# Performance work log

Hardware: AMD Instinct MI355X
Metric: run time of the kernel (lower is better)

Reference implementation:

```python
import jax, jax.numpy as jnp
import numpy as np
from jax import lax

INPUT_DIM = 16
H1 = 5
H2 = 50
NUM_CLASSES = 20
B = 4096
T = 512


def _lstm(x, w_ih, w_hh, b_ih, b_hh, hidden):
    # x: [B, T, D]; PyTorch LSTM gate order i, f, g, o; returns all hidden states [B, T, H]
    xg = jnp.einsum('btd,gd->btg', x, w_ih) + (b_ih + b_hh)  # [B, T, 4H]
    xg_t = jnp.swapaxes(xg, 0, 1)  # [T, B, 4H]
    h0 = jnp.zeros((x.shape[0], hidden), x.dtype)
    c0 = jnp.zeros((x.shape[0], hidden), x.dtype)

    def step(carry, xt):
        h, c = carry
        g = xt + h @ w_hh.T  # [B, 4H]
        i, f, gg, o = jnp.split(g, 4, axis=-1)
        i = jax.nn.sigmoid(i)
        f = jax.nn.sigmoid(f)
        gg = jnp.tanh(gg)
        o = jax.nn.sigmoid(o)
        c = f * c + i * gg
        h = o * jnp.tanh(c)
        return (h, c), h

    _, hs = lax.scan(step, (h0, c0), xg_t)
    return jnp.swapaxes(hs, 0, 1)  # [B, T, H]


def setup_inputs() -> dict:
    key = jax.random.key(0)
    ks = jax.random.split(key, 12)
    s1 = 1.0 / np.sqrt(H1)
    s2 = 1.0 / np.sqrt(H2)
    u = lambda k, shape, s: jax.random.uniform(k, shape, jnp.float32, -s, s)
    return {
        'x': jax.random.normal(ks[0], (B, T, INPUT_DIM), jnp.float32),
        'w_ih1': u(ks[1], (4 * H1, INPUT_DIM), s1),
        'w_hh1': u(ks[2], (4 * H1, H1), s1),
        'b_ih1': u(ks[3], (4 * H1,), s1),
        'b_hh1': u(ks[4], (4 * H1,), s1),
        'w_ih2': u(ks[5], (4 * H2, H1), s2),
        'w_hh2': u(ks[6], (4 * H2, H2), s2),
        'b_ih2': u(ks[7], (4 * H2,), s2),
        'b_hh2': u(ks[8], (4 * H2,), s2),
        'fc_w': u(ks[9], (NUM_CLASSES, H2), s2),
        'fc_b': u(ks[10], (NUM_CLASSES,), s2),
    }


def reference(x, w_ih1, w_hh1, b_ih1, b_hh1, w_ih2, w_hh2, b_ih2, b_hh2, fc_w, fc_b):
    h1 = _lstm(x, w_ih1, w_hh1, b_ih1, b_hh1, H1)   # [B, T, 5]
    h2 = _lstm(h1, w_ih2, w_hh2, b_ih2, b_hh2, H2)  # [B, T, 50]
    feat = h2[:, -1, :]  # last timestep; dropout is identity in eval mode
    out = feat @ fc_w.T + fc_b  # [B, num_classes]
    return (out, feat)
```

## Files before the change

### kernel.cpp

```cpp
#include <hip/hip_runtime.h>
#include <stdint.h>

#define B_TOTAL 4096
#define T_STEPS 512
#define IN_DIM 16
#define H1 5
#define H2 50
#define NCLS 20

typedef __attribute__((ext_vector_type(8))) short bf16x8;
typedef __attribute__((ext_vector_type(4))) float f32x4;

__device__ inline unsigned short f2bf(float x){
  unsigned int u = __float_as_uint(x);
  u += 0x7FFFu + ((u >> 16) & 1u);
  return (unsigned short)(u >> 16);
}
__device__ inline float bf2f(unsigned short h){ return __uint_as_float(((unsigned int)h) << 16); }

#define LOG2E 1.44269504f
__device__ inline float sigm(float x){
  float e = __builtin_amdgcn_exp2f(-LOG2E * x);
  return __builtin_amdgcn_rcpf(1.0f + e);
}
__device__ inline float tanh_(float x){
  float e = __builtin_amdgcn_exp2f((2.0f*LOG2E) * x);
  float r = __builtin_amdgcn_rcpf(1.0f + e);
  return fmaf(-2.0f, r, 1.0f);
}

__global__ __launch_bounds__(320) void lstm_fused_kernel(
    const float* __restrict__ x,
    const float* __restrict__ w_ih1, const float* __restrict__ w_hh1,
    const float* __restrict__ b_ih1, const float* __restrict__ b_hh1,
    const float* __restrict__ w_ih2, const float* __restrict__ w_hh2,
    const float* __restrict__ b_ih2, const float* __restrict__ b_hh2,
    const float* __restrict__ fc_w, const float* __restrict__ fc_b,
    float* __restrict__ out)
{
  const int tid  = threadIdx.x;
  const int lane = tid & 63;
  const int wave = tid >> 6;
  const int l15  = lane & 15;
  const int quad = lane >> 4;
  const int b0   = blockIdx.x * 16;

  __shared__ __align__(16) unsigned short a1_hi[2][16*40];
  __shared__ __align__(16) unsigned short a1_lo[2][16*40];
  __shared__ __align__(16) unsigned short a2_hi[2][16*72];
  __shared__ __align__(16) unsigned short a2_lo[2][16*72];
  __shared__ float h2f[16*52];

  bf16x8 Bh[4][2], Bl[4][2];
  float bias[4];
  float cst[4] = {0.f, 0.f, 0.f, 0.f};

  if (wave == 4) {
    bool valid = l15 < H1;
#pragma unroll
    for (int tt=0; tt<4; ++tt){
      int grow = tt*H1 + l15;
#pragma unroll
      for (int j=0;j<8;j++){
        int k = quad*8 + j;
        float w = 0.f;
        if (valid){
          if (k < IN_DIM)          w = w_ih1[grow*IN_DIM + k];
          else if (k < IN_DIM+H1)  w = w_hh1[grow*H1 + (k-IN_DIM)];
        }
        unsigned short h = f2bf(w), l = f2bf(w - bf2f(h));
        Bh[tt][0][j] = (short)h; Bl[tt][0][j] = (short)l;
        Bh[tt][1][j] = 0;        Bl[tt][1][j] = 0;
      }
      bias[tt] = valid ? (b_ih1[grow] + b_hh1[grow]) : 0.f;
    }
  } else {
    int cg = wave*16 + l15;
    bool valid = cg < H2;
#pragma unroll
    for (int tt=0; tt<4; ++tt){
      int grow = tt*H2 + cg;
#pragma unroll
      for (int kt=0; kt<2; ++kt){
#pragma unroll
        for (int j=0;j<8;j++){
          int k = kt*32 + quad*8 + j;
          float w = 0.f;
          if (valid){
            if (k < H2)          w = w_hh2[grow*H2 + k];
            else if (k < H2+H1)  w = w_ih2[grow*H1 + (k-H2)];
          }
          unsigned short h = f2bf(w), l = f2bf(w - bf2f(h));
          Bh[tt][kt][j] = (short)h; Bl[tt][kt][j] = (short)l;
        }
      }
      bias[tt] = valid ? (b_ih2[grow] + b_hh2[grow]) : 0.f;
    }
  }

  {
    unsigned short* p;
    p = &a1_hi[0][0]; for (int i=tid;i<2*16*40;i+=320) p[i]=0;
    p = &a1_lo[0][0]; for (int i=tid;i<2*16*40;i+=320) p[i]=0;
    p = &a2_hi[0][0]; for (int i=tid;i<2*16*72;i+=320) p[i]=0;
    p = &a2_lo[0][0]; for (int i=tid;i<2*16*72;i+=320) p[i]=0;
  }

  const int xb = lane >> 2;
  const int xd = (lane & 3) * 4;
  float4 xa = make_float4(0,0,0,0);
  if (wave == 4) {
    float4 x0 = *(const float4*)&x[((size_t)(b0+xb)*T_STEPS + 0)*IN_DIM + xd];
    uint2 uh, ul;
    unsigned short h0=f2bf(x0.x), h1v=f2bf(x0.y), h2v=f2bf(x0.z), h3=f2bf(x0.w);
    unsigned short l0=f2bf(x0.x-bf2f(h0)), l1=f2bf(x0.y-bf2f(h1v)),
                   l2=f2bf(x0.z-bf2f(h2v)), l3=f2bf(x0.w-bf2f(h3));
    uh.x = (unsigned)h0 | ((unsigned)h1v<<16); uh.y = (unsigned)h2v | ((unsigned)h3<<16);
    ul.x = (unsigned)l0 | ((unsigned)l1<<16);  ul.y = (unsigned)l2 | ((unsigned)l3<<16);
    *(uint2*)&a1_hi[0][xb*40 + xd] = uh;
    *(uint2*)&a1_lo[0][xb*40 + xd] = ul;
    xa = *(const float4*)&x[((size_t)(b0+xb)*T_STEPS + 1)*IN_DIM + xd];
  }

  for (int t=0; t<=T_STEPS; ++t){
    __syncthreads();
    const int rd = t & 1, wr = rd ^ 1;

    if (wave == 4){
      if (t < T_STEPS){
        float4 xn = make_float4(0,0,0,0);
        if (t+2 < T_STEPS)
          xn = *(const float4*)&x[((size_t)(b0+xb)*T_STEPS + (t+2))*IN_DIM + xd];

        bf16x8 ah = *(const bf16x8*)&a1_hi[rd][l15*40 + quad*8];
        bf16x8 al = *(const bf16x8*)&a1_lo[rd][l15*40 + quad*8];
        f32x4 acc[4];
#pragma unroll
        for (int tt=0; tt<4; ++tt){
          f32x4 a = {bias[tt], bias[tt], bias[tt], bias[tt]};
          a = __builtin_amdgcn_mfma_f32_16x16x32_bf16(ah, Bh[tt][0], a, 0,0,0);
          a = __builtin_amdgcn_mfma_f32_16x16x32_bf16(al, Bh[tt][0], a, 0,0,0);
          a = __builtin_amdgcn_mfma_f32_16x16x32_bf16(ah, Bl[tt][0], a, 0,0,0);
          acc[tt] = a;
        }
#pragma unroll
        for (int r=0;r<4;r++){
          float gi = sigm(acc[0][r]);
          float gf = sigm(acc[1][r]);
          float gg = tanh_(acc[2][r]);
          float go = sigm(acc[3][r]);
          cst[r] = gf*cst[r] + gi*gg;
          float h = go * tanh_(cst[r]);
          unsigned short hh = f2bf(h), hl = f2bf(h - bf2f(hh));
          int bb = quad*4 + r;
          if (l15 < H1){
            a1_hi[wr][bb*40 + IN_DIM + l15] = hh;
            a1_lo[wr][bb*40 + IN_DIM + l15] = hl;
            a2_hi[wr][bb*72 + H2 + l15] = hh;
            a2_lo[wr][bb*72 + H2 + l15] = hl;
          }
        }
        if (t+1 < T_STEPS){
          unsigned short h0=f2bf(xa.x), h1v=f2bf(xa.y), h2v=f2bf(xa.z), h3=f2bf(xa.w);
          unsigned short l0=f2bf(xa.x-bf2f(h0)), l1=f2bf(xa.y-bf2f(h1v)),
                         l2=f2bf(xa.z-bf2f(h2v)), l3=f2bf(xa.w-bf2f(h3));
          uint2 uh, ul;
          uh.x = (unsigned)h0 | ((unsigned)h1v<<16); uh.y = (unsigned)h2v | ((unsigned)h3<<16);
          ul.x = (unsigned)l0 | ((unsigned)l1<<16);  ul.y = (unsigned)l2 | ((unsigned)l3<<16);
          *(uint2*)&a1_hi[wr][xb*40 + xd] = uh;
          *(uint2*)&a1_lo[wr][xb*40 + xd] = ul;
        }
        xa = xn;
      }
    } else {
      if (t >= 1){
        const int cg = wave*16 + l15;
        bf16x8 ah0 = *(const bf16x8*)&a2_hi[rd][l15*72 +  0 + quad*8];
        bf16x8 al0 = *(const bf16x8*)&a2_lo[rd][l15*72 +  0 + quad*8];
        bf16x8 ah1 = *(const bf16x8*)&a2_hi[rd][l15*72 + 32 + quad*8];
        bf16x8 al1 = *(const bf16x8*)&a2_lo[rd][l15*72 + 32 + quad*8];
        f32x4 acc[4];
#pragma unroll
        for (int tt=0; tt<4; ++tt){
          f32x4 a = {bias[tt], bias[tt], bias[tt], bias[tt]};
          a = __builtin_amdgcn_mfma_f32_16x16x32_bf16(ah0, Bh[tt][0], a, 0,0,0);
          a = __builtin_amdgcn_mfma_f32_16x16x32_bf16(al0, Bh[tt][0], a, 0,0,0);
          a = __builtin_amdgcn_mfma_f32_16x16x32_bf16(ah0, Bl[tt][0], a, 0,0,0);
          a = __builtin_amdgcn_mfma_f32_16x16x32_bf16(ah1, Bh[tt][1], a, 0,0,0);
          a = __builtin_amdgcn_mfma_f32_16x16x32_bf16(al1, Bh[tt][1], a, 0,0,0);
          a = __builtin_amdgcn_mfma_f32_16x16x32_bf16(ah1, Bl[tt][1], a, 0,0,0);
          acc[tt] = a;
        }
#pragma unroll
        for (int r=0;r<4;r++){
          float gi = sigm(acc[0][r]);
          float gf = sigm(acc[1][r]);
          float gg = tanh_(acc[2][r]);
          float go = sigm(acc[3][r]);
          cst[r] = gf*cst[r] + gi*gg;
          float h = go * tanh_(cst[r]);
          unsigned short hh = f2bf(h), hl = f2bf(h - bf2f(hh));
          int bb = quad*4 + r;
          if (cg < H2){
            a2_hi[wr][bb*72 + cg] = hh;
            a2_lo[wr][bb*72 + cg] = hl;
            if (t == T_STEPS){
              out[(size_t)B_TOTAL*NCLS + (size_t)(b0+bb)*H2 + cg] = h;
              h2f[bb*52 + cg] = h;
            }
          }
        }
      }
    }
  }

  __syncthreads();
  {
    int b = tid / 20, o = tid % 20;
    float s = fc_b[o];
#pragma unroll 10
    for (int k=0;k<H2;k++) s += fc_w[o*H2+k] * h2f[b*52+k];
    out[(size_t)(b0+b)*NCLS + o] = s;
  }
}

extern "C" void kernel_launch(void* const* d_in, const int* in_sizes, int n_in,
                              void* d_out, int out_size, void* d_ws, size_t ws_size,
                              hipStream_t stream) {
  const float* x     = (const float*)d_in[0];
  const float* w_ih1 = (const float*)d_in[1];
  const float* w_hh1 = (const float*)d_in[2];
  const float* b_ih1 = (const float*)d_in[3];
  const float* b_hh1 = (const float*)d_in[4];
  const float* w_ih2 = (const float*)d_in[5];
  const float* w_hh2 = (const float*)d_in[6];
  const float* b_ih2 = (const float*)d_in[7];
  const float* b_hh2 = (const float*)d_in[8];
  const float* fc_w  = (const float*)d_in[9];
  const float* fc_b  = (const float*)d_in[10];
  float* out = (float*)d_out;

  lstm_fused_kernel<<<dim3(B_TOTAL/16), dim3(320), 0, stream>>>(
      x, w_ih1, w_hh1, b_ih1, b_hh1, w_ih2, w_hh2, b_ih2, b_hh2, fc_w, fc_b, out);
}
```

Baseline: 733.5 us.

## Split LSTM gate computation across 12 waves with two-phase barrier per step

Raises the block from 5 to 12 waves. Layer-2 gates are now split over two roles (i,f vs g,o) and layer-1 gates get one wave per gate, with activations exchanged through shared memory and two barriers per timestep instead of one double-buffered barrier. Input x is staged eight timesteps at a time into an LDS ring rather than loaded every step. Float-to-bf16 hi/lo splitting switches from round-to-nearest to truncation with byte-permute packing. The aim is a shorter per-step critical path on the serial recurrence, paid for by an extra barrier per step and more LDS traffic.

```diff
diff --git a/kernel.cpp b/kernel.cpp
--- a/kernel.cpp
+++ b/kernel.cpp
@@ -11,13 +11,6 @@
 typedef __attribute__((ext_vector_type(8))) short bf16x8;
 typedef __attribute__((ext_vector_type(4))) float f32x4;
 
-__device__ inline unsigned short f2bf(float x){
-  unsigned int u = __float_as_uint(x);
-  u += 0x7FFFu + ((u >> 16) & 1u);
-  return (unsigned short)(u >> 16);
-}
-__device__ inline float bf2f(unsigned short h){ return __uint_as_float(((unsigned int)h) << 16); }
-
 #define LOG2E 1.44269504f
 __device__ inline float sigm(float x){
   float e = __builtin_amdgcn_exp2f(-LOG2E * x);
@@ -28,8 +21,31 @@
   float r = __builtin_amdgcn_rcpf(1.0f + e);
   return fmaf(-2.0f, r, 1.0f);
 }
-
-__global__ __launch_bounds__(320) void lstm_fused_kernel(
+__device__ inline unsigned pack_top(float a, float b){
+  return __builtin_amdgcn_perm(__float_as_uint(a), __float_as_uint(b), 0x07060302u);
+}
+__device__ inline void cvt_store(unsigned short* dh, unsigned short* dl, float4 v){
+  unsigned x0=__float_as_uint(v.x), x1=__float_as_uint(v.y),
+           x2=__float_as_uint(v.z), x3=__float_as_uint(v.w);
+  uint2 H, L;
+  H.x = pack_top(v.y, v.x);
+  H.y = pack_top(v.w, v.z);
+  float r0 = v.x - __uint_as_float(x0 & 0xFFFF0000u);
+  float r1 = v.y - __uint_as_float(x1 & 0xFFFF0000u);
+  float r2 = v.z - __uint_as_float(x2 & 0xFFFF0000u);
+  float r3 = v.w - __uint_as_float(x3 & 0xFFFF0000u);
+  L.x = pack_top(r1, r0);
+  L.y = pack_top(r3, r2);
+  *(uint2*)dh = H; *(uint2*)dl = L;
+}
+__device__ inline void split1(float h, unsigned short& hi, unsigned short& lo){
+  unsigned u = __float_as_uint(h);
+  hi = (unsigned short)(u >> 16);
+  float r = h - __uint_as_float(u & 0xFFFF0000u);
+  lo = (unsigned short)(__float_as_uint(r) >> 16);
+}
+
+__global__ __launch_bounds__(768) void lstm_fused_kernel(
     const float* __restrict__ x,
     const float* __restrict__ w_ih1, const float* __restrict__ w_hh1,
     const float* __restrict__ b_ih1, const float* __restrict__ b_hh1,
@@ -45,177 +61,244 @@
   const int quad = lane >> 4;
   const int b0   = blockIdx.x * 16;
 
-  __shared__ __align__(16) unsigned short a1_hi[2][16*40];
-  __shared__ __align__(16) unsigned short a1_lo[2][16*40];
-  __shared__ __align__(16) unsigned short a2_hi[2][16*72];
-  __shared__ __align__(16) unsigned short a2_lo[2][16*72];
+  __shared__ __align__(16) unsigned short a2h[16*72], a2l[16*72];
+  __shared__ __align__(16) unsigned short a1h[16*24], a1l[16*24];
+  __shared__ __align__(16) unsigned short xrh[8*16*24], xrl[8*16*24];
+  __shared__ float g2[2*16*68];
+  __shared__ float g1[3*16*8 + 16];
   __shared__ float h2f[16*52];
 
-  bf16x8 Bh[4][2], Bl[4][2];
-  float bias[4];
-  float cst[4] = {0.f, 0.f, 0.f, 0.f};
-
-  if (wave == 4) {
-    bool valid = l15 < H1;
-#pragma unroll
-    for (int tt=0; tt<4; ++tt){
-      int grow = tt*H1 + l15;
-#pragma unroll
-      for (int j=0;j<8;j++){
-        int k = quad*8 + j;
-        float w = 0.f;
-        if (valid){
-          if (k < IN_DIM)          w = w_ih1[grow*IN_DIM + k];
-          else if (k < IN_DIM+H1)  w = w_hh1[grow*H1 + (k-IN_DIM)];
-        }
-        unsigned short h = f2bf(w), l = f2bf(w - bf2f(h));
-        Bh[tt][0][j] = (short)h; Bl[tt][0][j] = (short)l;
-        Bh[tt][1][j] = 0;        Bl[tt][1][j] = 0;
-      }
-      bias[tt] = valid ? (b_ih1[grow] + b_hh1[grow]) : 0.f;
-    }
-  } else {
-    int cg = wave*16 + l15;
+  bf16x8 Bh[2][2], Bl[2][2];
+  float bias0 = 0.f, bias1 = 0.f;
+  const bool is2  = wave < 8;
+  const int  grp  = wave & 3;
+  const int  role = wave >> 2;
+  const int  cg   = grp*16 + l15;
+
+  if (is2){
     bool valid = cg < H2;
 #pragma unroll
-    for (int tt=0; tt<4; ++tt){
+    for (int tl=0; tl<2; ++tl){
+      int tt = role*2 + tl;
       int grow = tt*H2 + cg;
 #pragma unroll
       for (int kt=0; kt<2; ++kt){
 #pragma unroll
         for (int j=0;j<8;j++){
-          int k = kt*32 + quad*8 + j;
+          int kk = kt*32 + quad*8 + j;
           float w = 0.f;
           if (valid){
-            if (k < H2)          w = w_hh2[grow*H2 + k];
-            else if (k < H2+H1)  w = w_ih2[grow*H1 + (k-H2)];
-          }
-          unsigned short h = f2bf(w), l = f2bf(w - bf2f(h));
-          Bh[tt][kt][j] = (short)h; Bl[tt][kt][j] = (short)l;
-        }
-      }
-      bias[tt] = valid ? (b_ih2[grow] + b_hh2[grow]) : 0.f;
-    }
+            if (kk < H2)         w = w_hh2[grow*H2 + kk];
+            else if (kk < H2+H1) w = w_ih2[grow*H1 + (kk-H2)];
+          }
+          unsigned u = __float_as_uint(w);
+          Bh[tl][kt][j] = (short)(u >> 16);
+          float r = w - __uint_as_float(u & 0xFFFF0000u);
+          Bl[tl][kt][j] = (short)(__float_as_uint(r) >> 16);
+        }
+      }
+      float bv = valid ? (b_ih2[grow] + b_hh2[grow]) : 0.f;
+      if (tl==0) bias0 = bv; else bias1 = bv;
+    }
+  } else {
+    int tt = wave & 3;
+    bool valid = l15 < H1;
+    int grow = tt*H1 + l15;
+#pragma unroll
+    for (int j=0;j<8;j++){
+      int kk = quad*8 + j;
+      float w = 0.f;
+      if (valid){
+        if (kk < IN_DIM)             w = w_ih1[grow*IN_DIM + kk];
+        else if (kk < IN_DIM+H1)     w = w_hh1[grow*H1 + (kk-IN_DIM)];
+      }
+      unsigned u = __float_as_uint(w);
+      Bh[0][0][j] = (short)(u >> 16);
+      float r = w - __uint_as_float(u & 0xFFFF0000u);
+      Bl[0][0][j] = (short)(__float_as_uint(r) >> 16);
+      Bh[0][1][j] = 0; Bl[0][1][j] = 0;
+      Bh[1][0][j] = 0; Bl[1][0][j] = 0;
+      Bh[1][1][j] = 0; Bl[1][1][j] = 0;
+    }
+    bias0 = valid ? (b_ih1[grow] + b_hh1[grow]) : 0.f;
   }
 
-  {
-    unsigned short* p;
-    p = &a1_hi[0][0]; for (int i=tid;i<2*16*40;i+=320) p[i]=0;
-    p = &a1_lo[0][0]; for (int i=tid;i<2*16*40;i+=320) p[i]=0;
-    p = &a2_hi[0][0]; for (int i=tid;i<2*16*72;i+=320) p[i]=0;
-    p = &a2_lo[0][0]; for (int i=tid;i<2*16*72;i+=320) p[i]=0;
-  }
+  for (int i=tid;i<16*72;i+=768){ a2h[i]=0; a2l[i]=0; }
+  for (int i=tid;i<16*24;i+=768){ a1h[i]=0; a1l[i]=0; }
 
   const int xb = lane >> 2;
   const int xd = (lane & 3) * 4;
-  float4 xa = make_float4(0,0,0,0);
-  if (wave == 4) {
-    float4 x0 = *(const float4*)&x[((size_t)(b0+xb)*T_STEPS + 0)*IN_DIM + xd];
-    uint2 uh, ul;
-    unsigned short h0=f2bf(x0.x), h1v=f2bf(x0.y), h2v=f2bf(x0.z), h3=f2bf(x0.w);
-    unsigned short l0=f2bf(x0.x-bf2f(h0)), l1=f2bf(x0.y-bf2f(h1v)),
-                   l2=f2bf(x0.z-bf2f(h2v)), l3=f2bf(x0.w-bf2f(h3));
-    uh.x = (unsigned)h0 | ((unsigned)h1v<<16); uh.y = (unsigned)h2v | ((unsigned)h3<<16);
-    ul.x = (unsigned)l0 | ((unsigned)l1<<16);  ul.y = (unsigned)l2 | ((unsigned)l3<<16);
-    *(uint2*)&a1_hi[0][xb*40 + xd] = uh;
-    *(uint2*)&a1_lo[0][xb*40 + xd] = ul;
-    xa = *(const float4*)&x[((size_t)(b0+xb)*T_STEPS + 1)*IN_DIM + xd];
+  if (wave == 10){
+#pragma unroll
+    for (int s=0;s<8;s++){
+      float4 v = *(const float4*)&x[((size_t)(b0+xb)*T_STEPS + s)*IN_DIM + xd];
+      cvt_store(&xrh[(s*16+xb)*24+xd], &xrl[(s*16+xb)*24+xd], v);
+    }
   }
+  __syncthreads();
+
+  float cst[4] = {0.f,0.f,0.f,0.f};
+  float x7x=0.f, x7y=0.f, x7z=0.f, x7w=0.f;
 
   for (int t=0; t<=T_STEPS; ++t){
+    f32x4 acc0 = {0,0,0,0}, acc1 = {0,0,0,0};
+    bool reload = false;
+
+    if (is2){
+      if (t >= 1){
+        const int rb = l15*72;
+        bf16x8 ah0 = *(const bf16x8*)&a2h[rb +      quad*8];
+        bf16x8 al0 = *(const bf16x8*)&a2l[rb +      quad*8];
+        bf16x8 ah1 = *(const bf16x8*)&a2h[rb + 32 + quad*8];
+        bf16x8 al1 = *(const bf16x8*)&a2l[rb + 32 + quad*8];
+        acc0 = (f32x4){bias0,bias0,bias0,bias0};
+        acc0 = __builtin_amdgcn_mfma_f32_16x16x32_bf16(ah0, Bh[0][0], acc0, 0,0,0);
+        acc0 = __builtin_amdgcn_mfma_f32_16x16x32_bf16(al0, Bh[0][0], acc0, 0,0,0);
+        acc0 = __builtin_amdgcn_mfma_f32_16x16x32_bf16(ah0, Bl[0][0], acc0, 0,0,0);
+        acc0 = __builtin_amdgcn_mfma_f32_16x16x32_bf16(ah1, Bh[0][1], acc0, 0,0,0);
+        acc0 = __builtin_amdgcn_mfma_f32_16x16x32_bf16(al1, Bh[0][1], acc0, 0,0,0);
+        acc0 = __builtin_amdgcn_mfma_f32_16x16x32_bf16(ah1, Bl[0][1], acc0, 0,0,0);
+        acc1 = (f32x4){bias1,bias1,bias1,bias1};
+        acc1 = __builtin_amdgcn_mfma_f32_16x16x32_bf16(ah0, Bh[1][0], acc1, 0,0,0);
+        acc1 = __builtin_amdgcn_mfma_f32_16x16x32_bf16(al0, Bh[1][0], acc1, 0,0,0);
+        acc1 = __builtin_amdgcn_mfma_f32_16x16x32_bf16(ah0, Bl[1][0], acc1, 0,0,0);
+        acc1 = __builtin_amdgcn_mfma_f32_16x16x32_bf16(ah1, Bh[1][1], acc1, 0,0,0);
+        acc1 = __builtin_amdgcn_mfma_f32_16x16x32_bf16(al1, Bh[1][1], acc1, 0,0,0);
+        acc1 = __builtin_amdgcn_mfma_f32_16x16x32_bf16(ah1, Bl[1][1], acc1, 0,0,0);
+        if (role == 0){
+#pragma unroll
+          for (int r=0;r<4;r++){ acc0[r] = sigm(acc0[r]); acc1[r] = sigm(acc1[r]); }
+        } else {
+#pragma unroll
+          for (int r=0;r<4;r++){
+            float g = tanh_(acc0[r]);
+            float o = sigm(acc1[r]);
+            int row = quad*4 + r;
+            g2[       row*68 + cg] = g;
+            g2[1088 + row*68 + cg] = o;
+          }
+        }
+      }
+    } else {
+      if (t < T_STEPS){
+        float4 xv0,xv1,xv2,xv3,xv4,xv5,xv6,xv7;
+        reload = (wave==10) && ((t & 7) == 7) && (t < T_STEPS-8);
+        if (reload){
+          const float* xp = &x[((size_t)(b0+xb)*T_STEPS + (t+1))*IN_DIM + xd];
+          xv0 = *(const float4*)(xp +  0*IN_DIM);
+          xv1 = *(const float4*)(xp +  1*IN_DIM);
+          xv2 = *(const float4*)(xp +  2*IN_DIM);
+          xv3 = *(const float4*)(xp +  3*IN_DIM);
+          xv4 = *(const float4*)(xp +  4*IN_DIM);
+          xv5 = *(const float4*)(xp +  5*IN_DIM);
+          xv6 = *(const float4*)(xp +  6*IN_DIM);
+          xv7 = *(const float4*)(xp +  7*IN_DIM);
+        }
+        const int slot = t & 7;
+        const unsigned short* ph;
+        const unsigned short* pl;
+        if (quad < 2){
+          int off = (slot*16 + l15)*24 + quad*8;
+          ph = &xrh[off]; pl = &xrl[off];
+        } else {
+          int off = l15*24 + (quad-2)*8;
+          ph = &a1h[off]; pl = &a1l[off];
+        }
+        bf16x8 ah = *(const bf16x8*)ph;
+        bf16x8 al = *(const bf16x8*)pl;
+        acc0 = (f32x4){bias0,bias0,bias0,bias0};
+        acc0 = __builtin_amdgcn_mfma_f32_16x16x32_bf16(ah, Bh[0][0], acc0, 0,0,0);
+        acc0 = __builtin_amdgcn_mfma_f32_16x16x32_bf16(al, Bh[0][0], acc0, 0,0,0);
+        acc0 = __builtin_amdgcn_mfma_f32_16x16x32_bf16(ah, Bl[0][0], acc0, 0,0,0);
+        int tt = wave & 3;
+        if (wave == 8){
+#pragma unroll
+          for (int r=0;r<4;r++) acc0[r] = sigm(acc0[r]);
+        } else {
+#pragma unroll
+          for (int r=0;r<4;r++){
+            float v = (tt==2) ? tanh_(acc0[r]) : sigm(acc0[r]);
+            if (l15 < 8) g1[(tt-1)*128 + (quad*4+r)*8 + l15] = v;
+          }
+        }
+        if (reload){
+          int base = ((t+1) & 7); (void)base;
+          cvt_store(&xrh[(0*16+xb)*24+xd], &xrl[(0*16+xb)*24+xd], xv0);
+          cvt_store(&xrh[(1*16+xb)*24+xd], &xrl[(1*16+xb)*24+xd], xv1);
+          cvt_store(&xrh[(2*16+xb)*24+xd], &xrl[(2*16+xb)*24+xd], xv2);
+          cvt_store(&xrh[(3*16+xb)*24+xd], &xrl[(3*16+xb)*24+xd], xv3);
+          cvt_store(&xrh[(4*16+xb)*24+xd], &xrl[(4*16+xb)*24+xd], xv4);
+          cvt_store(&xrh[(5*16+xb)*24+xd], &xrl[(5*16+xb)*24+xd], xv5);
+          cvt_store(&xrh[(6*16+xb)*24+xd], &xrl[(6*16+xb)*24+xd], xv6);
+          x7x = xv7.x; x7y = xv7.y; x7z = xv7.z; x7w = xv7.w;
+        }
+      }
+    }
+
     __syncthreads();
-    const int rd = t & 1, wr = rd ^ 1;
-
-    if (wave == 4){
-      if (t < T_STEPS){
-        float4 xn = make_float4(0,0,0,0);
-        if (t+2 < T_STEPS)
-          xn = *(const float4*)&x[((size_t)(b0+xb)*T_STEPS + (t+2))*IN_DIM + xd];
-
-        bf16x8 ah = *(const bf16x8*)&a1_hi[rd][l15*40 + quad*8];
-        bf16x8 al = *(const bf16x8*)&a1_lo[rd][l15*40 + quad*8];
-        f32x4 acc[4];
-#pragma unroll
-        for (int tt=0; tt<4; ++tt){
-          f32x4 a = {bias[tt], bias[tt], bias[tt], bias[tt]};
-          a = __builtin_amdgcn_mfma_f32_16x16x32_bf16(ah, Bh[tt][0], a, 0,0,0);
-          a = __builtin_amdgcn_mfma_f32_16x16x32_bf16(al, Bh[tt][0], a, 0,0,0);
-          a = __builtin_amdgcn_mfma_f32_16x16x32_bf16(ah, Bl[tt][0], a, 0,0,0);
-          acc[tt] = a;
-        }
+
+    if (is2){
+      if (role == 0 && t >= 1){
+        float gg[4], go[4];
 #pragma unroll
         for (int r=0;r<4;r++){
-          float gi = sigm(acc[0][r]);
-          float gf = sigm(acc[1][r]);
-          float gg = tanh_(acc[2][r]);
-          float go = sigm(acc[3][r]);
-          cst[r] = gf*cst[r] + gi*gg;
-          float h = go * tanh_(cst[r]);
-          unsigned short hh = f2bf(h), hl = f2bf(h - bf2f(hh));
-          int bb = quad*4 + r;
+          int row = quad*4 + r;
+          gg[r] = g2[       row*68 + cg];
+          go[r] = g2[1088 + row*68 + cg];
+        }
+#pragma unroll
+        for (int r=0;r<4;r++){
+          cst[r] = acc1[r]*cst[r] + acc0[r]*gg[r];
+          float h = go[r] * tanh_(cst[r]);
+          int row = quad*4 + r;
+          if (cg < H2){
+            unsigned short hh, hl;
+            split1(h, hh, hl);
+            a2h[row*72 + cg] = hh;
+            a2l[row*72 + cg] = hl;
+            if (t == T_STEPS){
+              out[(size_t)B_TOTAL*NCLS + (size_t)(b0+row)*H2 + cg] = h;
+              h2f[row*52 + cg] = h;
+            }
+          }
+        }
+      }
+    } else if (t < T_STEPS){
+      if (wave == 8){
+        int cc = (l15 < H1) ? l15 : 0;
+        float gf[4], gg[4], go[4];
+#pragma unroll
+        for (int r=0;r<4;r++){
+          int row = quad*4 + r;
+          gf[r] = g1[0*128 + row*8 + cc];
+          gg[r] = g1[1*128 + row*8 + cc];
+          go[r] = g1[2*128 + row*8 + cc];
+        }
+#pragma unroll
+        for (int r=0;r<4;r++){
+          cst[r] = gf[r]*cst[r] + acc0[r]*gg[r];
+          float h = go[r] * tanh_(cst[r]);
+          int row = quad*4 + r;
           if (l15 < H1){
-            a1_hi[wr][bb*40 + IN_DIM + l15] = hh;
-            a1_lo[wr][bb*40 + IN_DIM + l15] = hl;
-            a2_hi[wr][bb*72 + H2 + l15] = hh;
-            a2_lo[wr][bb*72 + H2 + l15] = hl;
-          }
-        }
-        if (t+1 < T_STEPS){
-          unsigned short h0=f2bf(xa.x), h1v=f2bf(xa.y), h2v=f2bf(xa.z), h3=f2bf(xa.w);
-          unsigned short l0=f2bf(xa.x-bf2f(h0)), l1=f2bf(xa.y-bf2f(h1v)),
-                         l2=f2bf(xa.z-bf2f(h2v)), l3=f2bf(xa.w-bf2f(h3));
-          uint2 uh, ul;
-          uh.x = (unsigned)h0 | ((unsigned)h1v<<16); uh.y = (unsigned)h2v | ((unsigned)h3<<16);
-          ul.x = (unsigned)l0 | ((unsigned)l1<<16);  ul.y = (unsigned)l2 | ((unsigned)l3<<16);
-          *(uint2*)&a1_hi[wr][xb*40 + xd] = uh;
-          *(uint2*)&a1_lo[wr][xb*40 + xd] = ul;
-        }
-        xa = xn;
-      }
-    } else {
-      if (t >= 1){
-        const int cg = wave*16 + l15;
-        bf16x8 ah0 = *(const bf16x8*)&a2_hi[rd][l15*72 +  0 + quad*8];
-        bf16x8 al0 = *(const bf16x8*)&a2_lo[rd][l15*72 +  0 + quad*8];
-        bf16x8 ah1 = *(const bf16x8*)&a2_hi[rd][l15*72 + 32 + quad*8];
-        bf16x8 al1 = *(const bf16x8*)&a2_lo[rd][l15*72 + 32 + quad*8];
-        f32x4 acc[4];
-#pragma unroll
-        for (int tt=0; tt<4; ++tt){
-          f32x4 a = {bias[tt], bias[tt], bias[tt], bias[tt]};
-          a = __builtin_amdgcn_mfma_f32_16x16x32_bf16(ah0, Bh[tt][0], a, 0,0,0);
-          a = __builtin_amdgcn_mfma_f32_16x16x32_bf16(al0, Bh[tt][0], a, 0,0,0);
-          a = __builtin_amdgcn_mfma_f32_16x16x32_bf16(ah0, Bl[tt][0], a, 0,0,0);
-          a = __builtin_amdgcn_mfma_f32_16x16x32_bf16(ah1, Bh[tt][1], a, 0,0,0);
-          a = __builtin_amdgcn_mfma_f32_16x16x32_bf16(al1, Bh[tt][1], a, 0,0,0);
-          a = __builtin_amdgcn_mfma_f32_16x16x32_bf16(ah1, Bl[tt][1], a, 0,0,0);
-          acc[tt] = a;
-        }
-#pragma unroll
-        for (int r=0;r<4;r++){
-          float gi = sigm(acc[0][r]);
-          float gf = sigm(acc[1][r]);
-          float gg = tanh_(acc[2][r]);
-          float go = sigm(acc[3][r]);
-          cst[r] = gf*cst[r] + gi*gg;
-          float h = go * tanh_(cst[r]);
-          unsigned short hh = f2bf(h), hl = f2bf(h - bf2f(hh));
-          int bb = quad*4 + r;
-          if (cg < H2){
-            a2_hi[wr][bb*72 + cg] = hh;
-            a2_lo[wr][bb*72 + cg] = hl;
-            if (t == T_STEPS){
-              out[(size_t)B_TOTAL*NCLS + (size_t)(b0+bb)*H2 + cg] = h;
-              h2f[bb*52 + cg] = h;
-            }
-          }
-        }
-      }
-    }
+            unsigned short hh, hl;
+            split1(h, hh, hl);
+            a1h[row*24 + cc] = hh;
+            a1l[row*24 + cc] = hl;
+            a2h[row*72 + H2 + cc] = hh;
+            a2l[row*72 + H2 + cc] = hl;
+          }
+        }
+      }
+      if (reload){
+        float4 v; v.x=x7x; v.y=x7y; v.z=x7z; v.w=x7w;
+        cvt_store(&xrh[(7*16+xb)*24+xd], &xrl[(7*16+xb)*24+xd], v);
+      }
+    }
+
+    __syncthreads();
   }
 
-  __syncthreads();
-  {
+  if (tid < 320){
     int b = tid / 20, o = tid % 20;
     float s = fc_b[o];
 #pragma unroll 10
@@ -240,6 +323,6 @@
   const float* fc_b  = (const float*)d_in[10];
   float* out = (float*)d_out;
 
-  lstm_fused_kernel<<<dim3(B_TOTAL/16), dim3(320), 0, stream>>>(
+  lstm_fused_kernel<<<dim3(B_TOTAL/16), dim3(768), 0, stream>>>(
       x, w_ih1, w_hh1, b_ih1, b_hh1, w_ih2, w_hh2, b_ih2, b_hh2, fc_w, fc_b, out);
 }
```

New measurement: 749.2 us. 2.1% more time.

## Replace per-step block barriers with LDS counter spin-waits between LSTM layer waves

Applied to the files above, without the earlier changes.

Replaces the per-timestep __syncthreads with producer/consumer LDS atomic counters, so the layer-1 wave and the layer-2 waves synchronize point-to-point and can run up to a step apart. Input x is now prefetched four steps at a time into an 8-slot LDS ring. bf16 hi/lo splitting switches from round-to-nearest to truncation via byte permutes. MFMA accumulations are split into two independent chains to shorten the dependency latency. The aim is less barrier stall and conversion ALU work on the serial recurrence path, at the cost of spin-loop overhead, subtle memory-ordering risk, and a slight change in rounding.

```diff
diff --git a/kernel.cpp b/kernel.cpp
--- a/kernel.cpp
+++ b/kernel.cpp
@@ -11,13 +11,6 @@
 typedef __attribute__((ext_vector_type(8))) short bf16x8;
 typedef __attribute__((ext_vector_type(4))) float f32x4;
 
-__device__ inline unsigned short f2bf(float x){
-  unsigned int u = __float_as_uint(x);
-  u += 0x7FFFu + ((u >> 16) & 1u);
-  return (unsigned short)(u >> 16);
-}
-__device__ inline float bf2f(unsigned short h){ return __uint_as_float(((unsigned int)h) << 16); }
-
 #define LOG2E 1.44269504f
 __device__ inline float sigm(float x){
   float e = __builtin_amdgcn_exp2f(-LOG2E * x);
@@ -28,8 +21,39 @@
   float r = __builtin_amdgcn_rcpf(1.0f + e);
   return fmaf(-2.0f, r, 1.0f);
 }
-
-__global__ __launch_bounds__(320) void lstm_fused_kernel(
+__device__ inline unsigned pack_top(float a, float b){
+  return __builtin_amdgcn_perm(__float_as_uint(a), __float_as_uint(b), 0x07060302u);
+}
+__device__ inline void cvt_store(unsigned short* dh, unsigned short* dl, float4 v){
+  uint2 H, L;
+  H.x = pack_top(v.y, v.x);
+  H.y = pack_top(v.w, v.z);
+  float r0 = v.x - __uint_as_float(__float_as_uint(v.x) & 0xFFFF0000u);
+  float r1 = v.y - __uint_as_float(__float_as_uint(v.y) & 0xFFFF0000u);
+  float r2 = v.z - __uint_as_float(__float_as_uint(v.z) & 0xFFFF0000u);
+  float r3 = v.w - __uint_as_float(__float_as_uint(v.w) & 0xFFFF0000u);
+  L.x = pack_top(r1, r0);
+  L.y = pack_top(r3, r2);
+  *(uint2*)dh = H; *(uint2*)dl = L;
+}
+__device__ inline void split1(float h, unsigned short& hi, unsigned short& lo){
+  unsigned u = __float_as_uint(h);
+  hi = (unsigned short)(u >> 16);
+  float r = h - __uint_as_float(u & 0xFFFF0000u);
+  lo = (unsigned short)(__float_as_uint(r) >> 16);
+}
+__device__ inline void wsplit(float w, short& hi, short& lo){
+  unsigned u = __float_as_uint(w);
+  hi = (short)(u >> 16);
+  float r = w - __uint_as_float(u & 0xFFFF0000u);
+  lo = (short)(__float_as_uint(r) >> 16);
+}
+__device__ inline void spin_ge(unsigned* p, unsigned tgt){
+  while (__hip_atomic_load(p, __ATOMIC_ACQUIRE, __HIP_MEMORY_SCOPE_WORKGROUP) < tgt)
+    __builtin_amdgcn_s_sleep(1);
+}
+
+__global__ __launch_bounds__(320, 1) void lstm_fused_kernel(
     const float* __restrict__ x,
     const float* __restrict__ w_ih1, const float* __restrict__ w_hh1,
     const float* __restrict__ b_ih1, const float* __restrict__ b_hh1,
@@ -45,172 +69,184 @@
   const int quad = lane >> 4;
   const int b0   = blockIdx.x * 16;
 
-  __shared__ __align__(16) unsigned short a1_hi[2][16*40];
-  __shared__ __align__(16) unsigned short a1_lo[2][16*40];
-  __shared__ __align__(16) unsigned short a2_hi[2][16*72];
-  __shared__ __align__(16) unsigned short a2_lo[2][16*72];
+  __shared__ __align__(16) unsigned short a2h[2][16*72], a2l[2][16*72];
+  __shared__ __align__(16) unsigned short xrh[8][16*24], xrl[8][16*24];
+  __shared__ __align__(16) unsigned short a1h[16*24], a1l[16*24];
   __shared__ float h2f[16*52];
+  __shared__ unsigned cnt1, cnt2;
 
   bf16x8 Bh[4][2], Bl[4][2];
   float bias[4];
-  float cst[4] = {0.f, 0.f, 0.f, 0.f};
-
-  if (wave == 4) {
+  float cst[4] = {0.f,0.f,0.f,0.f};
+  const int cg = wave*16 + l15;
+
+  if (wave < 4){
+    bool valid = cg < H2;
+#pragma unroll
+    for (int tt=0; tt<4; ++tt){
+      int grow = tt*H2 + cg;
+#pragma unroll
+      for (int kt=0; kt<2; ++kt){
+#pragma unroll
+        for (int j=0;j<8;j++){
+          int kk = kt*32 + quad*8 + j;
+          float w = 0.f;
+          if (valid){
+            if (kk < H2)         w = w_hh2[grow*H2 + kk];
+            else if (kk < H2+H1) w = w_ih2[grow*H1 + (kk-H2)];
+          }
+          short hi, lo; wsplit(w, hi, lo);
+          Bh[tt][kt][j] = hi; Bl[tt][kt][j] = lo;
+        }
+      }
+      bias[tt] = valid ? (b_ih2[grow] + b_hh2[grow]) : 0.f;
+    }
+  } else {
     bool valid = l15 < H1;
 #pragma unroll
     for (int tt=0; tt<4; ++tt){
       int grow = tt*H1 + l15;
 #pragma unroll
       for (int j=0;j<8;j++){
-        int k = quad*8 + j;
+        int kk = quad*8 + j;
         float w = 0.f;
         if (valid){
-          if (k < IN_DIM)          w = w_ih1[grow*IN_DIM + k];
-          else if (k < IN_DIM+H1)  w = w_hh1[grow*H1 + (k-IN_DIM)];
-        }
-        unsigned short h = f2bf(w), l = f2bf(w - bf2f(h));
-        Bh[tt][0][j] = (short)h; Bl[tt][0][j] = (short)l;
-        Bh[tt][1][j] = 0;        Bl[tt][1][j] = 0;
+          if (kk < IN_DIM)         w = w_ih1[grow*IN_DIM + kk];
+          else if (kk < IN_DIM+H1) w = w_hh1[grow*H1 + (kk-IN_DIM)];
+        }
+        short hi, lo; wsplit(w, hi, lo);
+        Bh[tt][0][j] = hi; Bl[tt][0][j] = lo;
+        Bh[tt][1][j] = 0;  Bl[tt][1][j] = 0;
       }
       bias[tt] = valid ? (b_ih1[grow] + b_hh1[grow]) : 0.f;
     }
-  } else {
-    int cg = wave*16 + l15;
-    bool valid = cg < H2;
-#pragma unroll
-    for (int tt=0; tt<4; ++tt){
-      int grow = tt*H2 + cg;
-#pragma unroll
-      for (int kt=0; kt<2; ++kt){
-#pragma unroll
-        for (int j=0;j<8;j++){
-          int k = kt*32 + quad*8 + j;
-          float w = 0.f;
-          if (valid){
-            if (k < H2)          w = w_hh2[grow*H2 + k];
-            else if (k < H2+H1)  w = w_ih2[grow*H1 + (k-H2)];
-          }
-          unsigned short h = f2bf(w), l = f2bf(w - bf2f(h));
-          Bh[tt][kt][j] = (short)h; Bl[tt][kt][j] = (short)l;
-        }
-      }
-      bias[tt] = valid ? (b_ih2[grow] + b_hh2[grow]) : 0.f;
-    }
-  }
-
-  {
-    unsigned short* p;
-    p = &a1_hi[0][0]; for (int i=tid;i<2*16*40;i+=320) p[i]=0;
-    p = &a1_lo[0][0]; for (int i=tid;i<2*16*40;i+=320) p[i]=0;
-    p = &a2_hi[0][0]; for (int i=tid;i<2*16*72;i+=320) p[i]=0;
-    p = &a2_lo[0][0]; for (int i=tid;i<2*16*72;i+=320) p[i]=0;
-  }
+  }
+
+  { unsigned short* p = &a2h[0][0]; for (int i=tid;i<2*16*72;i+=320) p[i]=0; }
+  { unsigned short* p = &a2l[0][0]; for (int i=tid;i<2*16*72;i+=320) p[i]=0; }
+  { unsigned short* p = &a1h[0];    for (int i=tid;i<16*24;i+=320)   p[i]=0; }
+  { unsigned short* p = &a1l[0];    for (int i=tid;i<16*24;i+=320)   p[i]=0; }
+  if (tid == 0){ cnt1 = 0; cnt2 = 0; }
 
   const int xb = lane >> 2;
   const int xd = (lane & 3) * 4;
-  float4 xa = make_float4(0,0,0,0);
-  if (wave == 4) {
-    float4 x0 = *(const float4*)&x[((size_t)(b0+xb)*T_STEPS + 0)*IN_DIM + xd];
-    uint2 uh, ul;
-    unsigned short h0=f2bf(x0.x), h1v=f2bf(x0.y), h2v=f2bf(x0.z), h3=f2bf(x0.w);
-    unsigned short l0=f2bf(x0.x-bf2f(h0)), l1=f2bf(x0.y-bf2f(h1v)),
-                   l2=f2bf(x0.z-bf2f(h2v)), l3=f2bf(x0.w-bf2f(h3));
-    uh.x = (unsigned)h0 | ((unsigned)h1v<<16); uh.y = (unsigned)h2v | ((unsigned)h3<<16);
-    ul.x = (unsigned)l0 | ((unsigned)l1<<16);  ul.y = (unsigned)l2 | ((unsigned)l3<<16);
-    *(uint2*)&a1_hi[0][xb*40 + xd] = uh;
-    *(uint2*)&a1_lo[0][xb*40 + xd] = ul;
-    xa = *(const float4*)&x[((size_t)(b0+xb)*T_STEPS + 1)*IN_DIM + xd];
-  }
-
-  for (int t=0; t<=T_STEPS; ++t){
-    __syncthreads();
-    const int rd = t & 1, wr = rd ^ 1;
-
-    if (wave == 4){
-      if (t < T_STEPS){
-        float4 xn = make_float4(0,0,0,0);
-        if (t+2 < T_STEPS)
-          xn = *(const float4*)&x[((size_t)(b0+xb)*T_STEPS + (t+2))*IN_DIM + xd];
-
-        bf16x8 ah = *(const bf16x8*)&a1_hi[rd][l15*40 + quad*8];
-        bf16x8 al = *(const bf16x8*)&a1_lo[rd][l15*40 + quad*8];
-        f32x4 acc[4];
-#pragma unroll
-        for (int tt=0; tt<4; ++tt){
-          f32x4 a = {bias[tt], bias[tt], bias[tt], bias[tt]};
-          a = __builtin_amdgcn_mfma_f32_16x16x32_bf16(ah, Bh[tt][0], a, 0,0,0);
-          a = __builtin_amdgcn_mfma_f32_16x16x32_bf16(al, Bh[tt][0], a, 0,0,0);
-          a = __builtin_amdgcn_mfma_f32_16x16x32_bf16(ah, Bl[tt][0], a, 0,0,0);
-          acc[tt] = a;
-        }
-#pragma unroll
-        for (int r=0;r<4;r++){
-          float gi = sigm(acc[0][r]);
-          float gf = sigm(acc[1][r]);
-          float gg = tanh_(acc[2][r]);
-          float go = sigm(acc[3][r]);
-          cst[r] = gf*cst[r] + gi*gg;
-          float h = go * tanh_(cst[r]);
-          unsigned short hh = f2bf(h), hl = f2bf(h - bf2f(hh));
-          int bb = quad*4 + r;
-          if (l15 < H1){
-            a1_hi[wr][bb*40 + IN_DIM + l15] = hh;
-            a1_lo[wr][bb*40 + IN_DIM + l15] = hl;
-            a2_hi[wr][bb*72 + H2 + l15] = hh;
-            a2_lo[wr][bb*72 + H2 + l15] = hl;
+  if (wave == 4){
+#pragma unroll
+    for (int s=0;s<8;s++){
+      float4 v = *(const float4*)&x[((size_t)(b0+xb)*T_STEPS + s)*IN_DIM + xd];
+      cvt_store(&xrh[s][xb*24+xd], &xrl[s][xb*24+xd], v);
+    }
+  }
+  __syncthreads();
+
+  if (wave == 4){
+    float4 pf0, pf1, pf2, pf3;
+    bool pend = false;
+    for (int s=0; s<T_STEPS; ++s){
+      if (s >= 2) spin_ge(&cnt2, 4u*(unsigned)(s-1));
+
+      if ((s & 3) == 0 && s+4 < T_STEPS){
+        const float* xp = &x[((size_t)(b0+xb)*T_STEPS + (s+4))*IN_DIM + xd];
+        pf0 = *(const float4*)(xp + 0*IN_DIM);
+        pf1 = *(const float4*)(xp + 1*IN_DIM);
+        pf2 = *(const float4*)(xp + 2*IN_DIM);
+        pf3 = *(const float4*)(xp + 3*IN_DIM);
+        pend = true;
+      }
+
+      const int slot = s & 7;
+      bf16x8 ah, al;
+      if (quad < 2){
+        ah = *(const bf16x8*)&xrh[slot][l15*24 + quad*8];
+        al = *(const bf16x8*)&xrl[slot][l15*24 + quad*8];
+      } else {
+        ah = *(const bf16x8*)&a1h[l15*24 + (quad-2)*8];
+        al = *(const bf16x8*)&a1l[l15*24 + (quad-2)*8];
+      }
+      f32x4 acc[4];
+#pragma unroll
+      for (int tt=0; tt<4; ++tt){
+        f32x4 cA = {bias[tt],bias[tt],bias[tt],bias[tt]};
+        cA = __builtin_amdgcn_mfma_f32_16x16x32_bf16(ah, Bh[tt][0], cA, 0,0,0);
+        f32x4 cB = {0.f,0.f,0.f,0.f};
+        cB = __builtin_amdgcn_mfma_f32_16x16x32_bf16(ah, Bl[tt][0], cB, 0,0,0);
+        cB = __builtin_amdgcn_mfma_f32_16x16x32_bf16(al, Bh[tt][0], cB, 0,0,0);
+        acc[tt] = cA + cB;
+      }
+#pragma unroll
+      for (int r=0;r<4;r++){
+        float gi = sigm(acc[0][r]);
+        float gf = sigm(acc[1][r]);
+        float gg = tanh_(acc[2][r]);
+        float go = sigm(acc[3][r]);
+        cst[r] = gf*cst[r] + gi*gg;
+        float h = go * tanh_(cst[r]);
+        if (l15 < H1){
+          unsigned short hh, hl; split1(h, hh, hl);
+          int row = quad*4 + r;
+          a1h[row*24 + l15] = hh;
+          a1l[row*24 + l15] = hl;
+          a2h[s&1][row*72 + H2 + l15] = hh;
+          a2l[s&1][row*72 + H2 + l15] = hl;
+        }
+      }
+      if ((s & 3) == 2 && pend){
+        cvt_store(&xrh[(s+2)&7][xb*24+xd], &xrl[(s+2)&7][xb*24+xd], pf0);
+        cvt_store(&xrh[(s+3)&7][xb*24+xd], &xrl[(s+3)&7][xb*24+xd], pf1);
+        cvt_store(&xrh[(s+4)&7][xb*24+xd], &xrl[(s+4)&7][xb*24+xd], pf2);
+        cvt_store(&xrh[(s+5)&7][xb*24+xd], &xrl[(s+5)&7][xb*24+xd], pf3);
+        pend = false;
+      }
+      __threadfence_block();
+      if (lane == 0) atomicAdd(&cnt1, 1u);
+    }
+  } else {
+    const bool act = cg < H2;
+    for (int t=0; t<T_STEPS; ++t){
+      spin_ge(&cnt1, (unsigned)(t+1));
+      if (t >= 1) spin_ge(&cnt2, 4u*(unsigned)t);
+      const int rd = t & 1, wr = rd ^ 1;
+
+      const int rb = l15*72;
+      bf16x8 ah0 = *(const bf16x8*)&a2h[rd][rb +      quad*8];
+      bf16x8 al0 = *(const bf16x8*)&a2l[rd][rb +      quad*8];
+      bf16x8 ah1 = *(const bf16x8*)&a2h[rd][rb + 32 + quad*8];
+      bf16x8 al1 = *(const bf16x8*)&a2l[rd][rb + 32 + quad*8];
+
+      f32x4 acc[4];
+#pragma unroll
+      for (int tt=0; tt<4; ++tt){
+        f32x4 cA = {bias[tt],bias[tt],bias[tt],bias[tt]};
+        cA = __builtin_amdgcn_mfma_f32_16x16x32_bf16(ah0, Bh[tt][0], cA, 0,0,0);
+        cA = __builtin_amdgcn_mfma_f32_16x16x32_bf16(al0, Bh[tt][0], cA, 0,0,0);
+        cA = __builtin_amdgcn_mfma_f32_16x16x32_bf16(ah0, Bl[tt][0], cA, 0,0,0);
+        f32x4 cB = {0.f,0.f,0.f,0.f};
+        cB = __builtin_amdgcn_mfma_f32_16x16x32_bf16(ah1, Bh[tt][1], cB, 0,0,0);
+        cB = __builtin_amdgcn_mfma_f32_16x16x32_bf16(al1, Bh[tt][1], cB, 0,0,0);
+        cB = __builtin_amdgcn_mfma_f32_16x16x32_bf16(ah1, Bl[tt][1], cB, 0,0,0);
+        acc[tt] = cA + cB;
+      }
+#pragma unroll
+      for (int r=0;r<4;r++){
+        float gi = sigm(acc[0][r]);
+        float gf = sigm(acc[1][r]);
+        float gg = tanh_(acc[2][r]);
+        float go = sigm(acc[3][r]);
+        cst[r] = gf*cst[r] + gi*gg;
+        float h = go * tanh_(cst[r]);
+        if (act){
+          unsigned short hh, hl; split1(h, hh, hl);
+          int row = quad*4 + r;
+          a2h[wr][row*72 + cg] = hh;
+          a2l[wr][row*72 + cg] = hl;
+          if (t == T_STEPS-1){
+            out[(size_t)B_TOTAL*NCLS + (size_t)(b0+row)*H2 + cg] = h;
+            h2f[row*52 + cg] = h;
           }
         }
-        if (t+1 < T_STEPS){
-          unsigned short h0=f2bf(xa.x), h1v=f2bf(xa.y), h2v=f2bf(xa.z), h3=f2bf(xa.w);
-          unsigned short l0=f2bf(xa.x-bf2f(h0)), l1=f2bf(xa.y-bf2f(h1v)),
-                         l2=f2bf(xa.z-bf2f(h2v)), l3=f2bf(xa.w-bf2f(h3));
-          uint2 uh, ul;
-          uh.x = (unsigned)h0 | ((unsigned)h1v<<16); uh.y = (unsigned)h2v | ((unsigned)h3<<16);
-          ul.x = (unsigned)l0 | ((unsigned)l1<<16);  ul.y = (unsigned)l2 | ((unsigned)l3<<16);
-          *(uint2*)&a1_hi[wr][xb*40 + xd] = uh;
-          *(uint2*)&a1_lo[wr][xb*40 + xd] = ul;
-        }
-        xa = xn;
-      }
-    } else {
-      if (t >= 1){
-        const int cg = wave*16 + l15;
-        bf16x8 ah0 = *(const bf16x8*)&a2_hi[rd][l15*72 +  0 + quad*8];
-        bf16x8 al0 = *(const bf16x8*)&a2_lo[rd][l15*72 +  0 + quad*8];
-        bf16x8 ah1 = *(const bf16x8*)&a2_hi[rd][l15*72 + 32 + quad*8];
-        bf16x8 al1 = *(const bf16x8*)&a2_lo[rd][l15*72 + 32 + quad*8];
-        f32x4 acc[4];
-#pragma unroll
-        for (int tt=0; tt<4; ++tt){
-          f32x4 a = {bias[tt], bias[tt], bias[tt], bias[tt]};
-          a = __builtin_amdgcn_mfma_f32_16x16x32_bf16(ah0, Bh[tt][0], a, 0,0,0);
-          a = __builtin_amdgcn_mfma_f32_16x16x32_bf16(al0, Bh[tt][0], a, 0,0,0);
-          a = __builtin_amdgcn_mfma_f32_16x16x32_bf16(ah0, Bl[tt][0], a, 0,0,0);
-          a = __builtin_amdgcn_mfma_f32_16x16x32_bf16(ah1, Bh[tt][1], a, 0,0,0);
-          a = __builtin_amdgcn_mfma_f32_16x16x32_bf16(al1, Bh[tt][1], a, 0,0,0);
-          a = __builtin_amdgcn_mfma_f32_16x16x32_bf16(ah1, Bl[tt][1], a, 0,0,0);
-          acc[tt] = a;
-        }
-#pragma unroll
-        for (int r=0;r<4;r++){
-          float gi = sigm(acc[0][r]);
-          float gf = sigm(acc[1][r]);
-          float gg = tanh_(acc[2][r]);
-          float go = sigm(acc[3][r]);
-          cst[r] = gf*cst[r] + gi*gg;
-          float h = go * tanh_(cst[r]);
-          unsigned short hh = f2bf(h), hl = f2bf(h - bf2f(hh));
-          int bb = quad*4 + r;
-          if (cg < H2){
-            a2_hi[wr][bb*72 + cg] = hh;
-            a2_lo[wr][bb*72 + cg] = hl;
-            if (t == T_STEPS){
-              out[(size_t)B_TOTAL*NCLS + (size_t)(b0+bb)*H2 + cg] = h;
-              h2f[bb*52 + cg] = h;
-            }
-          }
-        }
-      }
+      }
+      __threadfence_block();
+      if (lane == 0) atomicAdd(&cnt2, 1u);
     }
   }
 
```

Result: slower. 758.1 us (+3.4%).
